# Kernel optimization log

Measured on AMD Instinct MI355X. Metric: run time of the kernel, lower is better.

## Reference

```python
import jax, jax.numpy as jnp
import numpy as np

N, E, B = 50000, 400000, 64
N_INC, E_OUTC, U_INC, G_INC = 64, 64, 32, 64
H1A, H1B = 128, 64           # node_model_mlp1_hidden_sizes
H2 = 256                     # node_model_mlp2_hidden_sizes[0]
DIM_LH, DIM_L, N_OUTC = 128, 32, 64
LN_EPS = 1e-5

def _lin_init(key, din, dout):
    k1, k2 = jax.random.split(key)
    bound = 1.0 / np.sqrt(din)
    W = jax.random.uniform(k1, (din, dout), jnp.float32, -bound, bound)
    b = jax.random.uniform(k2, (dout,), jnp.float32, -bound, bound)
    return W, b

def setup_inputs() -> dict:
    key = jax.random.key(0)
    ks = jax.random.split(key, 16)
    x = jax.random.normal(ks[0], (N, N_INC), jnp.float32)
    edge_index = jax.random.randint(ks[1], (2, E), 0, N, jnp.int64)
    edge_attr = jax.random.normal(ks[2], (E, E_OUTC), jnp.float32)
    u = jax.random.normal(ks[3], (B, U_INC), jnp.float32)
    batch = jnp.sort(jax.random.randint(ks[4], (N,), 0, B, jnp.int64))
    goal = jax.random.normal(ks[5], (N, G_INC), jnp.float32)
    W1, b1 = _lin_init(ks[6], N_INC + E_OUTC, H1A)
    g1, be1 = jnp.ones((H1A,), jnp.float32), jnp.zeros((H1A,), jnp.float32)
    W2, b2 = _lin_init(ks[7], H1A, H1B)
    mlp2_inc = N_INC + H1B + U_INC
    W3, b3 = _lin_init(ks[8], mlp2_inc, H2)
    g3, be3 = jnp.ones((H2,), jnp.float32), jnp.zeros((H2,), jnp.float32)
    W4, b4 = _lin_init(ks[9], H2, DIM_LH)
    g4, be4 = jnp.ones((DIM_LH,), jnp.float32), jnp.zeros((DIM_LH,), jnp.float32)
    Wm, bm = _lin_init(ks[10], DIM_LH, DIM_L)
    Wv, bv = _lin_init(ks[11], DIM_LH, DIM_L)
    Wx, bx = _lin_init(ks[12], DIM_L, N_OUTC)
    return dict(x=x, edge_index=edge_index, edge_attr=edge_attr, u=u, batch=batch,
                goal=goal, W1=W1, b1=b1, g1=g1, be1=be1, W2=W2, b2=b2,
                W3=W3, b3=b3, g3=g3, be3=be3, W4=W4, b4=b4, g4=g4, be4=be4,
                Wm=Wm, bm=bm, Wv=Wv, bv=bv, Wx=Wx, bx=bx)

def _layernorm(h, g, b):
    mu = jnp.mean(h, axis=-1, keepdims=True)
    var = jnp.var(h, axis=-1, keepdims=True)
    return (h - mu) * jax.lax.rsqrt(var + LN_EPS) * g + b

def reference(x, edge_index, edge_attr, u, batch, goal,
              W1, b1, g1, be1, W2, b2,
              W3, b3, g3, be3, W4, b4, g4, be4,
              Wm, bm, Wv, bv, Wx, bx):
    row, col = edge_index[0], edge_index[1]
    # --- edge MLP: gather x[row], concat edge_attr, 2-layer MLP with LN+ReLU
    se = jnp.concatenate([x[row], edge_attr], axis=1)          # [E, n_inc+e_outc]
    h = jax.nn.relu(_layernorm(se @ W1 + b1, g1, be1)) @ W2 + b2  # [E, H1B]
    # --- scatter_mean over destination nodes
    sums = jax.ops.segment_sum(h, col, num_segments=N)          # [N, H1B]
    cnts = jax.ops.segment_sum(jnp.ones((E,), h.dtype), col, num_segments=N)
    aggs = sums / jnp.maximum(cnts, 1.0)[:, None]
    # --- node MLP 2
    z = jnp.concatenate([x, aggs, u[batch]], axis=1)            # [N, mlp2_inc]
    z = jax.nn.relu(_layernorm(z @ W3 + b3, g3, be3))
    z = jax.nn.relu(_layernorm(z @ W4 + b4, g4, be4))           # [N, DIM_LH]
    z_mu = z @ Wm + bm
    z_var = z @ Wv + bv                                         # log-variance
    eps = jax.random.normal(jax.random.key(42), z_mu.shape, z_mu.dtype)
    z_s = z_mu + eps * jnp.exp(0.5 * z_var)                     # reparameterize
    out = z_s @ Wx + bx                                         # [N, n_outc]
    return (out, z_mu, z_var)
```

## Files before the change

### kernel.cpp

```cpp
#include <hip/hip_runtime.h>

#define NN 50000
#define EE 400000
#define NB 49

typedef __attribute__((ext_vector_type(8))) short bf16x8;
typedef __attribute__((ext_vector_type(4))) float f32x4;

__device__ __forceinline__ void fma4(float4& a, float s, const float4& w){
  a.x = fmaf(s, w.x, a.x);
  a.y = fmaf(s, w.y, a.y);
  a.z = fmaf(s, w.z, a.z);
  a.w = fmaf(s, w.w, a.w);
}

__device__ __forceinline__ unsigned short f2bf(float f){
  unsigned u = __float_as_uint(f);
  unsigned r = (u + 0x7fffu + ((u >> 16) & 1u)) >> 16;
  return (unsigned short)r;
}

__device__ __forceinline__ bf16x8 cvt8(float4 lo, float4 hi){
  bf16x8 r;
  r[0]=(short)f2bf(lo.x); r[1]=(short)f2bf(lo.y); r[2]=(short)f2bf(lo.z); r[3]=(short)f2bf(lo.w);
  r[4]=(short)f2bf(hi.x); r[5]=(short)f2bf(hi.y); r[6]=(short)f2bf(hi.z); r[7]=(short)f2bf(hi.w);
  return r;
}

__device__ __forceinline__ unsigned rotl32(unsigned v, int d){ return (v<<d)|(v>>(32-d)); }

__device__ __forceinline__ float eps_at(unsigned idx){
  const unsigned k0 = 0u, k1 = 42u, k2 = 0x1BD11BDAu ^ 0u ^ 42u;
  unsigned x0 = 0u + k0, x1 = idx + k1;
  const int rotA[4] = {13,15,26,6};
  const int rotB[4] = {17,29,16,24};
  #pragma unroll
  for (int i=0;i<4;i++){ x0 += x1; x1 = rotl32(x1, rotA[i]); x1 ^= x0; }
  x0 += k1; x1 += k2 + 1u;
  #pragma unroll
  for (int i=0;i<4;i++){ x0 += x1; x1 = rotl32(x1, rotB[i]); x1 ^= x0; }
  x0 += k2; x1 += k0 + 2u;
  #pragma unroll
  for (int i=0;i<4;i++){ x0 += x1; x1 = rotl32(x1, rotA[i]); x1 ^= x0; }
  x0 += k0; x1 += k1 + 3u;
  #pragma unroll
  for (int i=0;i<4;i++){ x0 += x1; x1 = rotl32(x1, rotB[i]); x1 ^= x0; }
  x0 += k1; x1 += k2 + 4u;
  #pragma unroll
  for (int i=0;i<4;i++){ x0 += x1; x1 = rotl32(x1, rotA[i]); x1 ^= x0; }
  x0 += k2; x1 += k0 + 5u;
  unsigned bits = x0 ^ x1;
  float f = __uint_as_float((bits >> 9) | 0x3f800000u) - 1.0f;
  const float lo = -0.99999994f;
  float u = f * 2.0f + lo;
  u = fmaxf(u, lo);
  float w = -log1pf(-u*u);
  float p;
  if (w < 5.0f){
    w -= 2.5f;
    p = 2.81022636e-08f;
    p = fmaf(p,w, 3.43273939e-07f);
    p = fmaf(p,w,-3.5233877e-06f);
    p = fmaf(p,w,-4.39150654e-06f);
    p = fmaf(p,w, 0.00021858087f);
    p = fmaf(p,w,-0.00125372503f);
    p = fmaf(p,w,-0.00417768164f);
    p = fmaf(p,w, 0.246640727f);
    p = fmaf(p,w, 1.50140941f);
  } else {
    w = sqrtf(w) - 3.0f;
    p = -0.000200214257f;
    p = fmaf(p,w, 0.000100950558f);
    p = fmaf(p,w, 0.00134934322f);
    p = fmaf(p,w,-0.00367342844f);
    p = fmaf(p,w, 0.00573950773f);
    p = fmaf(p,w,-0.0076224613f);
    p = fmaf(p,w, 0.00943887047f);
    p = fmaf(p,w, 1.00167406f);
    p = fmaf(p,w, 2.83297682f);
  }
  return 1.41421356237f * (p * u);
}

__global__ __launch_bounds__(256) void k_prep_x(const float* __restrict__ x,
                                                unsigned short* __restrict__ xb){
  int t = blockIdx.x*256 + threadIdx.x;
  if (t < NN*64/8){
    const float4* p = (const float4*)(x + t*8);
    bf16x8 v = cvt8(p[0], p[1]);
    *(bf16x8*)(xb + t*8) = v;
  }
}

__global__ __launch_bounds__(256) void k_prep_w(const float* __restrict__ W1,
                                                const float* __restrict__ W2,
                                                unsigned short* __restrict__ W1T,
                                                unsigned short* __restrict__ W2T){
  for (int i = threadIdx.x; i < 128*128; i += 256){
    int n = i >> 7, k = i & 127;
    W1T[i] = f2bf(W1[k*128 + n]);
  }
  for (int i = threadIdx.x; i < 64*128; i += 256){
    int n = i >> 7, k = i & 127;
    W2T[i] = f2bf(W2[k*64 + n]);
  }
}

__global__ __launch_bounds__(256) void k_hist(const int* __restrict__ ei, int* __restrict__ cnt){
  int e = blockIdx.x*256 + threadIdx.x;
  if (e < EE) atomicAdd(&cnt[ei[EE + e]], 1);
}

__global__ __launch_bounds__(256) void k_scan1(const int* __restrict__ cnt,
                                               int* __restrict__ offs,
                                               int* __restrict__ partials){
  __shared__ int sdata[256];
  const int t = threadIdx.x, b = blockIdx.x;
  const int base = b*1024 + t*4;
  int v0 = (base+0 < NN) ? cnt[base+0] : 0;
  int v1 = (base+1 < NN) ? cnt[base+1] : 0;
  int v2 = (base+2 < NN) ? cnt[base+2] : 0;
  int v3 = (base+3 < NN) ? cnt[base+3] : 0;
  int tsum = v0+v1+v2+v3;
  sdata[t] = tsum;
  __syncthreads();
  for (int off=1; off<256; off<<=1){
    int add = (t >= off) ? sdata[t-off] : 0;
    __syncthreads();
    sdata[t] += add;
    __syncthreads();
  }
  int run = sdata[t] - tsum;
  if (base+0 < NN) offs[base+0] = run;  run += v0;
  if (base+1 < NN) offs[base+1] = run;  run += v1;
  if (base+2 < NN) offs[base+2] = run;  run += v2;
  if (base+3 < NN) offs[base+3] = run;
  if (t == 255) partials[b] = sdata[255];
}

__global__ __launch_bounds__(64) void k_scan2(int* __restrict__ partials){
  int l = threadIdx.x;
  int v = (l < NB) ? partials[l] : 0;
  int inc = v;
  #pragma unroll
  for (int off=1; off<64; off<<=1){
    int t = __shfl_up(inc, off);
    if (l >= off) inc += t;
  }
  if (l < NB) partials[l] = inc - v;
}

__global__ __launch_bounds__(256) void k_scan3(int* __restrict__ offs,
                                               const int* __restrict__ partials,
                                               int* __restrict__ cursor){
  const int t = threadIdx.x, b = blockIdx.x;
  const int base = b*1024 + t*4;
  int add = partials[b];
  #pragma unroll
  for (int k=0;k<4;k++){
    int i = base + k;
    if (i < NN){ int o = offs[i] + add; offs[i] = o; cursor[i] = o; }
  }
}

__global__ __launch_bounds__(256) void k_fill(const int* __restrict__ ei,
                                              int* __restrict__ cursor,
                                              int* __restrict__ eidx){
  int e = blockIdx.x*256 + threadIdx.x;
  if (e < EE){
    int c = ei[EE + e];
    int pos = atomicAdd(&cursor[c], 1);
    eidx[pos] = e;
  }
}

#define H1STR 132
__global__ __launch_bounds__(256, 4) void k_edge(const int* __restrict__ ei,
    const float* __restrict__ ea,
    const unsigned short* __restrict__ xb,
    const unsigned short* __restrict__ W1T, const float* __restrict__ b1,
    const float* __restrict__ g1, const float* __restrict__ be1,
    const unsigned short* __restrict__ W2T, const float* __restrict__ b2,
    float* __restrict__ h_ws){
  __shared__ __align__(16) float h1[64*H1STR];
  __shared__ int rows_l[64];
  const int tid  = threadIdx.x;
  const int base = blockIdx.x * 64;
  const int wv   = tid >> 6;
  const int lane = tid & 63;
  const int quad = lane >> 4;
  const int l16  = lane & 15;
  if (tid < 64) rows_l[tid] = ei[base + tid];
  __syncthreads();
  {
    int rw[4];
    #pragma unroll
    for (int m=0;m<4;m++) rw[m] = rows_l[m*16 + l16];
    f32x4 acc[4][2];
    #pragma unroll
    for (int m=0;m<4;m++){ acc[m][0] = (f32x4){0.f,0.f,0.f,0.f}; acc[m][1] = (f32x4){0.f,0.f,0.f,0.f}; }
    #pragma unroll
    for (int ks=0; ks<4; ks++){
      bf16x8 af[4];
      if (ks < 2){
        #pragma unroll
        for (int m=0;m<4;m++)
          af[m] = *(const bf16x8*)(xb + (size_t)rw[m]*64 + ks*32 + quad*8);
      } else {
        #pragma unroll
        for (int m=0;m<4;m++){
          const float* p = ea + (size_t)(base + m*16 + l16)*64 + (ks-2)*32 + quad*8;
          af[m] = cvt8(*(const float4*)p, *(const float4*)(p+4));
        }
      }
      bf16x8 bf0 = *(const bf16x8*)(W1T + (size_t)((2*wv+0)*16 + l16)*128 + ks*32 + quad*8);
      bf16x8 bf1 = *(const bf16x8*)(W1T + (size_t)((2*wv+1)*16 + l16)*128 + ks*32 + quad*8);
      #pragma unroll
      for (int m=0;m<4;m++){
        acc[m][0] = __builtin_amdgcn_mfma_f32_16x16x32_bf16(af[m], bf0, acc[m][0], 0, 0, 0);
        acc[m][1] = __builtin_amdgcn_mfma_f32_16x16x32_bf16(af[m], bf1, acc[m][1], 0, 0, 0);
      }
    }
    #pragma unroll
    for (int nl=0; nl<2; nl++){
      float b1c = b1[(2*wv+nl)*16 + l16];
      #pragma unroll
      for (int m=0;m<4;m++){
        #pragma unroll
        for (int r=0;r<4;r++)
          h1[(m*16 + quad*4 + r)*H1STR + (2*wv+nl)*16 + l16] = acc[m][nl][r] + b1c;
      }
    }
  }
  __syncthreads();
  {
    const float gA = g1[lane], gB = g1[lane+64];
    const float bA = be1[lane], bB = be1[lane+64];
    for (int r = wv*16; r < wv*16 + 16; ++r){
      float a = h1[r*H1STR + lane];
      float b = h1[r*H1STR + 64 + lane];
      float s = a + b, ss = fmaf(a,a,b*b);
      #pragma unroll
      for (int off=32; off; off>>=1){
        s  += __shfl_xor(s, off);
        ss += __shfl_xor(ss, off);
      }
      float mean = s * (1.0f/128.0f);
      float var  = ss * (1.0f/128.0f) - mean*mean;
      float inv = rsqrtf(var + 1e-5f);
      h1[r*H1STR + lane]      = fmaxf(fmaf((a-mean)*inv, gA, bA), 0.f);
      h1[r*H1STR + 64 + lane] = fmaxf(fmaf((b-mean)*inv, gB, bB), 0.f);
    }
  }
  __syncthreads();
  {
    f32x4 acc2[4];
    #pragma unroll
    for (int m=0;m<4;m++) acc2[m] = (f32x4){0.f,0.f,0.f,0.f};
    #pragma unroll
    for (int ks=0; ks<4; ks++){
      bf16x8 bfr = *(const bf16x8*)(W2T + (size_t)(wv*16 + l16)*128 + ks*32 + quad*8);
      #pragma unroll
      for (int m=0;m<4;m++){
        const float* p = h1 + (m*16 + l16)*H1STR + ks*32 + quad*8;
        bf16x8 af = cvt8(*(const float4*)p, *(const float4*)(p+4));
        acc2[m] = __builtin_amdgcn_mfma_f32_16x16x32_bf16(af, bfr, acc2[m], 0, 0, 0);
      }
    }
    float b2c = b2[wv*16 + l16];
    #pragma unroll
    for (int m=0;m<4;m++){
      #pragma unroll
      for (int r=0;r<4;r++)
        h_ws[(size_t)(base + m*16 + quad*4 + r)*64 + wv*16 + l16] = acc2[m][r] + b2c;
    }
  }
}

#define T2STR 132
#define ZSSTR 36
__global__ __launch_bounds__(256, 3) void k_node(const float* __restrict__ x,
    const float* __restrict__ u, const int* __restrict__ batch,
    const float* __restrict__ h_ws, const int* __restrict__ cnt,
    const int* __restrict__ offs, const int* __restrict__ eidx,
    const float* __restrict__ W3, const float* __restrict__ b3,
    const float* __restrict__ g3, const float* __restrict__ be3,
    const float* __restrict__ W4, const float* __restrict__ b4,
    const float* __restrict__ g4, const float* __restrict__ be4,
    const float* __restrict__ Wm, const float* __restrict__ bm,
    const float* __restrict__ Wv, const float* __restrict__ bv,
    const float* __restrict__ Wx, const float* __restrict__ bx,
    float* __restrict__ out){
  __shared__ __align__(16) float zS[32*160];
  __shared__ __align__(16) float h3S[32*256];
  const int tid = threadIdx.x;
  const int base = blockIdx.x * 32;
  #pragma unroll
  for (int i=0;i<2;i++){
    int l = tid + 256*i;
    int r = l >> 4, c4 = (l & 15) * 4;
    int n = base + r;
    float4 v = make_float4(0.f,0.f,0.f,0.f);
    if (n < NN) v = *(const float4*)(x + (size_t)n*64 + c4);
    *(float4*)(zS + r*160 + c4) = v;
  }
  {
    int r = tid >> 3, c4 = (tid & 7) * 4;
    int n = base + r;
    float4 v = make_float4(0.f,0.f,0.f,0.f);
    if (n < NN) v = *(const float4*)(u + (size_t)batch[n]*32 + c4);
    *(float4*)(zS + r*160 + 128 + c4) = v;
  }
  {
    int r = tid >> 3, p = tid & 7;
    int n = base + r;
    float4 a0 = make_float4(0.f,0.f,0.f,0.f), a1 = a0;
    int deg = 0;
    if (n < NN){
      deg = cnt[n];
      int start = offs[n];
      for (int j=0;j<deg;j++){
        int e = eidx[start + j];
        const float* hp = h_ws + (size_t)e*64 + p*8;
        float4 v0 = *(const float4*)(hp);
        float4 v1 = *(const float4*)(hp + 4);
        a0.x += v0.x; a0.y += v0.y; a0.z += v0.z; a0.w += v0.w;
        a1.x += v1.x; a1.y += v1.y; a1.z += v1.z; a1.w += v1.w;
      }
    }
    float rc = 1.0f / fmaxf((float)deg, 1.0f);
    a0.x*=rc; a0.y*=rc; a0.z*=rc; a0.w*=rc;
    a1.x*=rc; a1.y*=rc; a1.z*=rc; a1.w*=rc;
    *(float4*)(zS + r*160 + 64 + p*8)     = a0;
    *(float4*)(zS + r*160 + 64 + p*8 + 4) = a1;
  }
  __syncthreads();
  {
    const int jq = tid & 63, rb = tid >> 6;
    float4 acc[8];
    #pragma unroll
    for (int r=0;r<8;r++) acc[r] = make_float4(0.f,0.f,0.f,0.f);
    for (int k=0;k<160;k+=4){
      float4 w0 = *(const float4*)(W3 + (k+0)*256 + 4*jq);
      float4 w1 = *(const float4*)(W3 + (k+1)*256 + 4*jq);
      float4 w2 = *(const float4*)(W3 + (k+2)*256 + 4*jq);
      float4 w3v= *(const float4*)(W3 + (k+3)*256 + 4*jq);
      #pragma unroll
      for (int r=0;r<8;r++){
        float4 z = *(const float4*)(zS + (rb*8+r)*160 + k);
        fma4(acc[r], z.x, w0); fma4(acc[r], z.y, w1);
        fma4(acc[r], z.z, w2); fma4(acc[r], z.w, w3v);
      }
    }
    float4 bb  = *(const float4*)(b3 + 4*jq);
    float4 gg  = *(const float4*)(g3 + 4*jq);
    float4 bet = *(const float4*)(be3 + 4*jq);
    #pragma unroll
    for (int r=0;r<8;r++){
      float4 v = acc[r];
      v.x += bb.x; v.y += bb.y; v.z += bb.z; v.w += bb.w;
      float s  = v.x + v.y + v.z + v.w;
      float ss = fmaf(v.x,v.x, fmaf(v.y,v.y, fmaf(v.z,v.z, v.w*v.w)));
      #pragma unroll
      for (int off=32; off; off>>=1){ s += __shfl_xor(s,off); ss += __shfl_xor(ss,off); }
      float mean = s * (1.0f/256.0f);
      float inv  = rsqrtf(ss*(1.0f/256.0f) - mean*mean + 1e-5f);
      float4 o;
      o.x = fmaxf(fmaf((v.x-mean)*inv, gg.x, bet.x), 0.f);
      o.y = fmaxf(fmaf((v.y-mean)*inv, gg.y, bet.y), 0.f);
      o.z = fmaxf(fmaf((v.z-mean)*inv, gg.z, bet.z), 0.f);
      o.w = fmaxf(fmaf((v.w-mean)*inv, gg.w, bet.w), 0.f);
      *(float4*)(h3S + (rb*8+r)*256 + 4*jq) = o;
    }
  }
  __syncthreads();
  {
    const int jq = tid & 31, rb = tid >> 5;
    float4 acc[4];
    #pragma unroll
    for (int r=0;r<4;r++) acc[r] = make_float4(0.f,0.f,0.f,0.f);
    for (int k=0;k<256;k+=4){
      float4 w0 = *(const float4*)(W4 + (k+0)*128 + 4*jq);
      float4 w1 = *(const float4*)(W4 + (k+1)*128 + 4*jq);
      float4 w2 = *(const float4*)(W4 + (k+2)*128 + 4*jq);
      float4 w3 = *(const float4*)(W4 + (k+3)*128 + 4*jq);
      #pragma unroll
      for (int r=0;r<4;r++){
        float4 z = *(const float4*)(h3S + (rb*4+r)*256 + k);
        fma4(acc[r], z.x, w0); fma4(acc[r], z.y, w1);
        fma4(acc[r], z.z, w2); fma4(acc[r], z.w, w3);
      }
    }
    float4 bb  = *(const float4*)(b4 + 4*jq);
    float4 gg  = *(const float4*)(g4 + 4*jq);
    float4 bet = *(const float4*)(be4 + 4*jq);
    #pragma unroll
    for (int r=0;r<4;r++){
      float4 v = acc[r];
      v.x += bb.x; v.y += bb.y; v.z += bb.z; v.w += bb.w;
      float s  = v.x + v.y + v.z + v.w;
      float ss = fmaf(v.x,v.x, fmaf(v.y,v.y, fmaf(v.z,v.z, v.w*v.w)));
      #pragma unroll
      for (int off=16; off; off>>=1){ s += __shfl_xor(s,off); ss += __shfl_xor(ss,off); }
      float mean = s * (1.0f/128.0f);
      float inv  = rsqrtf(ss*(1.0f/128.0f) - mean*mean + 1e-5f);
      float4 o;
      o.x = fmaxf(fmaf((v.x-mean)*inv, gg.x, bet.x), 0.f);
      o.y = fmaxf(fmaf((v.y-mean)*inv, gg.y, bet.y), 0.f);
      o.z = fmaxf(fmaf((v.z-mean)*inv, gg.z, bet.z), 0.f);
      o.w = fmaxf(fmaf((v.w-mean)*inv, gg.w, bet.w), 0.f);
      *(float4*)(zS + (rb*4+r)*T2STR + 4*jq) = o;
    }
  }
  __syncthreads();
  {
    const int jq = tid & 15, rb = tid >> 4;
    const float* Wp = (jq < 8) ? Wm : Wv;
    const int cq = (jq & 7) * 4;
    float4 acc[2];
    #pragma unroll
    for (int r=0;r<2;r++) acc[r] = make_float4(0.f,0.f,0.f,0.f);
    for (int k=0;k<128;k+=4){
      float4 w0 = *(const float4*)(Wp + (k+0)*32 + cq);
      float4 w1 = *(const float4*)(Wp + (k+1)*32 + cq);
      float4 w2 = *(const float4*)(Wp + (k+2)*32 + cq);
      float4 w3 = *(const float4*)(Wp + (k+3)*32 + cq);
      #pragma unroll
      for (int r=0;r<2;r++){
        float4 z = *(const float4*)(zS + (rb*2+r)*T2STR + k);
        fma4(acc[r], z.x, w0); fma4(acc[r], z.y, w1);
        fma4(acc[r], z.z, w2); fma4(acc[r], z.w, w3);
      }
    }
    const float* bp = (jq < 8) ? bm : bv;
    float4 bb = *(const float4*)(bp + cq);
    const long long sec = (jq < 8) ? (long long)NN*64 : ((long long)NN*64 + (long long)NN*32);
    #pragma unroll
    for (int r=0;r<2;r++){
      float4 v = acc[r];
      v.x += bb.x; v.y += bb.y; v.z += bb.z; v.w += bb.w;
      int rr = rb*2 + r;
      *(float4*)(h3S + rr*64 + ((jq<8)?0:32) + cq) = v;
      int n = base + rr;
      if (n < NN) *(float4*)(out + sec + (long long)n*32 + cq) = v;
    }
  }
  __syncthreads();
  #pragma unroll
  for (int i=0;i<4;i++){
    int l = tid + 256*i;
    int r = l >> 5, jj = l & 31;
    float mu = h3S[r*64 + jj];
    float lv = h3S[r*64 + 32 + jj];
    unsigned idx = (unsigned)((base + r)*32 + jj);
    float e = eps_at(idx);
    zS[r*ZSSTR + jj] = fmaf(e, expf(0.5f*lv), mu);
  }
  __syncthreads();
  {
    const int jq = tid & 15, rb = tid >> 4;
    float4 acc[2];
    #pragma unroll
    for (int r=0;r<2;r++) acc[r] = make_float4(0.f,0.f,0.f,0.f);
    for (int k=0;k<32;k+=4){
      float4 w0 = *(const float4*)(Wx + (k+0)*64 + 4*jq);
      float4 w1 = *(const float4*)(Wx + (k+1)*64 + 4*jq);
      float4 w2 = *(const float4*)(Wx + (k+2)*64 + 4*jq);
      float4 w3 = *(const float4*)(Wx + (k+3)*64 + 4*jq);
      #pragma unroll
      for (int r=0;r<2;r++){
        float4 z = *(const float4*)(zS + (rb*2+r)*ZSSTR + k);
        fma4(acc[r], z.x, w0); fma4(acc[r], z.y, w1);
        fma4(acc[r], z.z, w2); fma4(acc[r], z.w, w3);
      }
    }
    float4 bb = *(const float4*)(bx + 4*jq);
    #pragma unroll
    for (int r=0;r<2;r++){
      int n = base + rb*2 + r;
      if (n < NN){
        float4 v = acc[r];
        v.x += bb.x; v.y += bb.y; v.z += bb.z; v.w += bb.w;
        *(float4*)(out + (long long)n*64 + 4*jq) = v;
      }
    }
  }
}

extern "C" void kernel_launch(void* const* d_in, const int* in_sizes, int n_in,
                              void* d_out, int out_size, void* d_ws, size_t ws_size,
                              hipStream_t stream) {
  const float* x     = (const float*)d_in[0];
  const int*   ei    = (const int*)d_in[1];
  const float* ea    = (const float*)d_in[2];
  const float* u     = (const float*)d_in[3];
  const int*   batch = (const int*)d_in[4];
  const float* W1 = (const float*)d_in[6];
  const float* b1 = (const float*)d_in[7];
  const float* g1 = (const float*)d_in[8];
  const float* be1= (const float*)d_in[9];
  const float* W2 = (const float*)d_in[10];
  const float* b2 = (const float*)d_in[11];
  const float* W3 = (const float*)d_in[12];
  const float* b3 = (const float*)d_in[13];
  const float* g3 = (const float*)d_in[14];
  const float* be3= (const float*)d_in[15];
  const float* W4 = (const float*)d_in[16];
  const float* b4 = (const float*)d_in[17];
  const float* g4 = (const float*)d_in[18];
  const float* be4= (const float*)d_in[19];
  const float* Wm = (const float*)d_in[20];
  const float* bm = (const float*)d_in[21];
  const float* Wv = (const float*)d_in[22];
  const float* bv = (const float*)d_in[23];
  const float* Wx = (const float*)d_in[24];
  const float* bx = (const float*)d_in[25];

  char* W = (char*)d_ws;
  size_t off = 0;
  float* h_ws = (float*)(W + off);  off += (size_t)EE*64*4;
  int* cnt      = (int*)(W + off);  off += (size_t)NN*4;
  int* offs     = (int*)(W + off);  off += (size_t)NN*4;
  int* cursor   = (int*)(W + off);  off += (size_t)NN*4;
  int* eidx     = (int*)(W + off);  off += (size_t)EE*4;
  int* partials = (int*)(W + off);  off += 256;
  unsigned short* xb  = (unsigned short*)(W + off); off += (size_t)NN*64*2;
  unsigned short* W1T = (unsigned short*)(W + off); off += 128*128*2;
  unsigned short* W2T = (unsigned short*)(W + off); off += 64*128*2;
  float* out = (float*)d_out;

  hipMemsetAsync(cnt, 0, (size_t)NN*sizeof(int), stream);

  k_prep_x<<<(NN*64/8 + 255)/256, 256, 0, stream>>>(x, xb);
  k_prep_w<<<1, 256, 0, stream>>>(W1, W2, W1T, W2T);
  k_hist <<<(EE+255)/256, 256, 0, stream>>>(ei, cnt);
  k_scan1<<<NB, 256, 0, stream>>>(cnt, offs, partials);
  k_scan2<<<1, 64, 0, stream>>>(partials);
  k_scan3<<<NB, 256, 0, stream>>>(offs, partials, cursor);
  k_fill <<<(EE+255)/256, 256, 0, stream>>>(ei, cursor, eidx);

  k_edge<<<EE/64, 256, 0, stream>>>(ei, ea, xb, W1T, b1, g1, be1, W2T, b2, h_ws);
  k_node<<<(NN+31)/32, 256, 0, stream>>>(x, u, batch, h_ws, cnt, offs, eidx,
                                         W3,b3,g3,be3, W4,b4,g4,be4,
                                         Wm,bm, Wv,bv, Wx,bx, out);
}
```

Baseline: 585.7 us.

## Scatter edge outputs into CSR-sorted order so node aggregation reads contiguously

The fill kernel now records each edge's destination slot in CSR order, and the edge kernel writes its MLP output rows straight to that slot instead of to the edge index. The node kernel can then sum a contiguous run of h rows per node without the indirect eidx lookup, and the loop is unrolled by two. This removes one level of indirection and makes the aggregation reads sequential, in exchange for scattered 256-byte row writes from the edge kernel.

```diff
diff --git a/kernel.cpp b/kernel.cpp
--- a/kernel.cpp
+++ b/kernel.cpp
@@ -165,12 +165,11 @@
 
 __global__ __launch_bounds__(256) void k_fill(const int* __restrict__ ei,
                                               int* __restrict__ cursor,
-                                              int* __restrict__ eidx){
+                                              int* __restrict__ epos){
   int e = blockIdx.x*256 + threadIdx.x;
   if (e < EE){
     int c = ei[EE + e];
-    int pos = atomicAdd(&cursor[c], 1);
-    eidx[pos] = e;
+    epos[e] = atomicAdd(&cursor[c], 1);
   }
 }
 
@@ -181,9 +180,11 @@
     const unsigned short* __restrict__ W1T, const float* __restrict__ b1,
     const float* __restrict__ g1, const float* __restrict__ be1,
     const unsigned short* __restrict__ W2T, const float* __restrict__ b2,
+    const int* __restrict__ epos,
     float* __restrict__ h_ws){
   __shared__ __align__(16) float h1[64*H1STR];
   __shared__ int rows_l[64];
+  __shared__ int slot_l[64];
   const int tid  = threadIdx.x;
   const int base = blockIdx.x * 64;
   const int wv   = tid >> 6;
@@ -191,6 +192,7 @@
   const int quad = lane >> 4;
   const int l16  = lane & 15;
   if (tid < 64) rows_l[tid] = ei[base + tid];
+  if (tid >= 128 && tid < 192) slot_l[tid-128] = epos[base + tid - 128];
   __syncthreads();
   {
     int rw[4];
@@ -272,7 +274,7 @@
     for (int m=0;m<4;m++){
       #pragma unroll
       for (int r=0;r<4;r++)
-        h_ws[(size_t)(base + m*16 + quad*4 + r)*64 + wv*16 + l16] = acc2[m][r] + b2c;
+        h_ws[(size_t)slot_l[m*16 + quad*4 + r]*64 + wv*16 + l16] = acc2[m][r] + b2c;
     }
   }
 }
@@ -282,7 +284,7 @@
 __global__ __launch_bounds__(256, 3) void k_node(const float* __restrict__ x,
     const float* __restrict__ u, const int* __restrict__ batch,
     const float* __restrict__ h_ws, const int* __restrict__ cnt,
-    const int* __restrict__ offs, const int* __restrict__ eidx,
+    const int* __restrict__ offs,
     const float* __restrict__ W3, const float* __restrict__ b3,
     const float* __restrict__ g3, const float* __restrict__ be3,
     const float* __restrict__ W4, const float* __restrict__ b4,
@@ -318,10 +320,20 @@
     int deg = 0;
     if (n < NN){
       deg = cnt[n];
-      int start = offs[n];
-      for (int j=0;j<deg;j++){
-        int e = eidx[start + j];
-        const float* hp = h_ws + (size_t)e*64 + p*8;
+      const float* hp = h_ws + (size_t)offs[n]*64 + p*8;
+      int j = 0;
+      for (; j + 2 <= deg; j += 2){
+        float4 v0 = *(const float4*)(hp);
+        float4 v1 = *(const float4*)(hp + 4);
+        float4 w0 = *(const float4*)(hp + 64);
+        float4 w1 = *(const float4*)(hp + 68);
+        hp += 128;
+        a0.x += v0.x; a0.y += v0.y; a0.z += v0.z; a0.w += v0.w;
+        a1.x += v1.x; a1.y += v1.y; a1.z += v1.z; a1.w += v1.w;
+        a0.x += w0.x; a0.y += w0.y; a0.z += w0.z; a0.w += w0.w;
+        a1.x += w1.x; a1.y += w1.y; a1.z += w1.z; a1.w += w1.w;
+      }
+      if (j < deg){
         float4 v0 = *(const float4*)(hp);
         float4 v1 = *(const float4*)(hp + 4);
         a0.x += v0.x; a0.y += v0.y; a0.z += v0.z; a0.w += v0.w;
@@ -522,7 +534,7 @@
   int* cnt      = (int*)(W + off);  off += (size_t)NN*4;
   int* offs     = (int*)(W + off);  off += (size_t)NN*4;
   int* cursor   = (int*)(W + off);  off += (size_t)NN*4;
-  int* eidx     = (int*)(W + off);  off += (size_t)EE*4;
+  int* epos     = (int*)(W + off);  off += (size_t)EE*4;
   int* partials = (int*)(W + off);  off += 256;
   unsigned short* xb  = (unsigned short*)(W + off); off += (size_t)NN*64*2;
   unsigned short* W1T = (unsigned short*)(W + off); off += 128*128*2;
@@ -537,10 +549,10 @@
   k_scan1<<<NB, 256, 0, stream>>>(cnt, offs, partials);
   k_scan2<<<1, 64, 0, stream>>>(partials);
   k_scan3<<<NB, 256, 0, stream>>>(offs, partials, cursor);
-  k_fill <<<(EE+255)/256, 256, 0, stream>>>(ei, cursor, eidx);
-
-  k_edge<<<EE/64, 256, 0, stream>>>(ei, ea, xb, W1T, b1, g1, be1, W2T, b2, h_ws);
-  k_node<<<(NN+31)/32, 256, 0, stream>>>(x, u, batch, h_ws, cnt, offs, eidx,
+  k_fill <<<(EE+255)/256, 256, 0, stream>>>(ei, cursor, epos);
+
+  k_edge<<<EE/64, 256, 0, stream>>>(ei, ea, xb, W1T, b1, g1, be1, W2T, b2, epos, h_ws);
+  k_node<<<(NN+31)/32, 256, 0, stream>>>(x, u, batch, h_ws, cnt, offs,
                                          W3,b3,g3,be3, W4,b4,g4,be4,
                                          Wm,bm, Wv,bv, Wx,bx, out);
 }
```

Measured after the change: 575.0 us. Within noise of the previous version (-1.8%).
